# Performance work log

Hardware: AMD Instinct MI355X
Metric: run time of the kernel (lower is better)

## Reference

```python
import jax, jax.numpy as jnp
import numpy as np

N, B, LMAX, M, D, KV, H = 12288, 4, 4096, 1024, 256, 512, 8
EPS = 1e-5


def layernorm(x, g, b):
    mu = jnp.mean(x, axis=-1, keepdims=True)
    var = jnp.mean(jnp.square(x - mu), axis=-1, keepdims=True)
    return (x - mu) * jax.lax.rsqrt(var + EPS) * g + b


def setup_inputs() -> dict:
    key = jax.random.key(0)
    ks = jax.random.split(key, 8)
    s = 0.02
    F = jax.random.normal(ks[0], (N, D), jnp.float32)
    batch_idx = jnp.sort(jax.random.randint(ks[1], (N,), 0, B, dtype=jnp.int32))
    y = jax.random.normal(ks[2], (B, M, KV), jnp.float32)
    Wq = jax.random.normal(ks[3], (D, D), jnp.float32) * s
    Wk = jax.random.normal(ks[4], (D, KV), jnp.float32) * s
    Wv = jax.random.normal(ks[5], (D, KV), jnp.float32) * s
    Wo = jax.random.normal(ks[6], (D, D), jnp.float32) * s
    zb = jnp.zeros((D,), jnp.float32)
    return dict(F=F, batch_idx=batch_idx, y=y,
                Wq=Wq, bq=zb, Wk=Wk, bk=zb, Wv=Wv, bv=zb, Wo=Wo, bo=zb,
                ln_g=jnp.ones((D,), jnp.float32), ln_b=zb, Lmax=LMAX)


def reference(F, batch_idx, y, Wq, bq, Wk, bk, Wv, bv, Wo, bo, ln_g, ln_b, Lmax):
    Bn, Mn, _ = y.shape
    n, d = F.shape
    # sparse_to_dense: scatter points into [B, Lmax, D] by (batch, position-in-batch)
    counts = jax.ops.segment_sum(jnp.ones((n,), jnp.int32), batch_idx, num_segments=Bn)
    starts = jnp.cumsum(counts) - counts                      # first row of each batch
    pos = jnp.arange(n, dtype=jnp.int32) - starts[batch_idx]  # intra-batch position
    xd = jnp.zeros((Bn, Lmax, d), F.dtype).at[batch_idx, pos].set(F)
    # pre-norm (shared LayerNorm params, reused again post-residual)
    q_in = layernorm(xd, ln_g, ln_b)
    # multi-head cross-attention (no key padding mask: mask arg is None here)
    dh = d // H
    q = (q_in @ Wq.T + bq).reshape(Bn, Lmax, H, dh)
    k = (y @ Wk.T + bk).reshape(Bn, Mn, H, dh)
    v = (y @ Wv.T + bv).reshape(Bn, Mn, H, dh)
    scores = jnp.einsum('blhd,bmhd->bhlm', q, k) / jnp.sqrt(jnp.float32(dh))
    p = jax.nn.softmax(scores, axis=-1)
    o = jnp.einsum('bhlm,bmhd->blhd', p, v).reshape(Bn, Lmax, d)
    attn = o @ Wo.T + bo
    # residual on the (normed) query, then the SAME LayerNorm again
    res = layernorm(q_in + attn, ln_g, ln_b)
    # dense_to_sparse: gather valid rows back (row-major order == input order)
    return res[batch_idx, pos]
```

## Files before the change

### kernel.cpp

```cpp
#include <hip/hip_runtime.h>

constexpr int NP = 12288;
constexpr int NB = 4;
constexpr int MC = 1024;
constexpr int DM = 256;
constexpr int KVD = 512;
constexpr int NH = 8;
constexpr int DH = 32;

typedef __bf16 bf16x8 __attribute__((ext_vector_type(8)));
typedef __bf16 bf16x4 __attribute__((ext_vector_type(4)));
typedef float f32x4v __attribute__((ext_vector_type(4)));

__device__ inline bf16x8 pack8(float4 a, float4 b) {
    bf16x8 r;
    r[0] = (__bf16)a.x; r[1] = (__bf16)a.y; r[2] = (__bf16)a.z; r[3] = (__bf16)a.w;
    r[4] = (__bf16)b.x; r[5] = (__bf16)b.y; r[6] = (__bf16)b.z; r[7] = (__bf16)b.w;
    return r;
}

__global__ __launch_bounds__(256) void k_prep(const float* __restrict__ F,
        const int* __restrict__ bidx,
        const float* __restrict__ wq, const float* __restrict__ wk,
        const float* __restrict__ wv, const float* __restrict__ wo,
        const float* __restrict__ g, const float* __restrict__ bb,
        int* __restrict__ starts,
        __bf16* wqb, __bf16* wkb, __bf16* wvb, __bf16* wob,
        __bf16* __restrict__ q_in_b) {
    const int bid = blockIdx.x, t = threadIdx.x;
    if (bid == 0) {
        if (t > NB) return;
        int lo = 0, hi = NP;
        while (lo < hi) { int mid = (lo + hi) >> 1; if (bidx[mid] < t) lo = mid + 1; else hi = mid; }
        starts[t] = lo;
        return;
    }
    if (bid <= 384) {
        size_t i = ((size_t)(bid - 1) * 256 + t) * 4;
        const float* s; __bf16* d; size_t off;
        if      (i < 65536)  { s = wq; d = wqb; off = 0; }
        else if (i < 196608) { s = wk; d = wkb; off = 65536; }
        else if (i < 327680) { s = wv; d = wvb; off = 196608; }
        else                 { s = wo; d = wob; off = 327680; }
        size_t j = i - off;
        float4 v = *(const float4*)&s[j];
        bf16x4 o; o[0] = (__bf16)v.x; o[1] = (__bf16)v.y; o[2] = (__bf16)v.z; o[3] = (__bf16)v.w;
        *(bf16x4*)&d[j] = o;
        return;
    }
    const int w = t >> 6, l = t & 63;
    size_t row = (size_t)(bid - 385) * 4 + w;
    float4 v = *(const float4*)&F[row * DM + l * 4];
    float s = v.x + v.y + v.z + v.w;
#pragma unroll
    for (int o2 = 1; o2 < 64; o2 <<= 1) s += __shfl_xor(s, o2);
    float mu = s * (1.f / DM);
    float4 d = {v.x - mu, v.y - mu, v.z - mu, v.w - mu};
    float ss = d.x * d.x + d.y * d.y + d.z * d.z + d.w * d.w;
#pragma unroll
    for (int o2 = 1; o2 < 64; o2 <<= 1) ss += __shfl_xor(ss, o2);
    float rr = rsqrtf(ss * (1.f / DM) + 1e-5f);
    float4 gg = *(const float4*)&g[l * 4];
    float4 bv = *(const float4*)&bb[l * 4];
    bf16x4 ob4;
    ob4[0] = (__bf16)(d.x * rr * gg.x + bv.x);
    ob4[1] = (__bf16)(d.y * rr * gg.y + bv.y);
    ob4[2] = (__bf16)(d.z * rr * gg.z + bv.z);
    ob4[3] = (__bf16)(d.w * rr * gg.w + bv.w);
    *(bf16x4*)&q_in_b[row * DM + l * 4] = ob4;
}

__global__ __launch_bounds__(256) void k_qkv(const __bf16* __restrict__ Aq,
        const __bf16* __restrict__ Wq, const float* __restrict__ bq,
        const float* __restrict__ Yf,
        const __bf16* __restrict__ Wk, const float* __restrict__ bk,
        const __bf16* __restrict__ Wv, const float* __restrict__ bv,
        __bf16* __restrict__ Qo, __bf16* __restrict__ Kp,
        __bf16* __restrict__ VpT, float qscale) {
    __shared__ __bf16 As[128][68];
    __shared__ __bf16 Bs[64][68];
    const int t = threadIdx.x;
    const int w = t >> 6, l = t & 63, lg = l >> 4, ln = l & 15;
    const int wr = w >> 1, wc = w & 1;
    const int ar = t >> 3, ac8 = (t & 7) * 8;
    if ((int)blockIdx.x < 384) {
        f32x4v acc[4][2] = {};
        const int K = DM;
        const int col0 = (blockIdx.x & 3) * 64, row0 = (blockIdx.x >> 2) * 128;
        bf16x8 ra0, ra1, ra2, ra3, rb0, rb1;
#define LOADGQ(K0) \
        ra0 = *(const bf16x8*)&Aq[(size_t)(row0 + ar) * K + (K0) + ac8];        \
        ra1 = *(const bf16x8*)&Aq[(size_t)(row0 + ar + 32) * K + (K0) + ac8];   \
        ra2 = *(const bf16x8*)&Aq[(size_t)(row0 + ar + 64) * K + (K0) + ac8];   \
        ra3 = *(const bf16x8*)&Aq[(size_t)(row0 + ar + 96) * K + (K0) + ac8];   \
        rb0 = *(const bf16x8*)&Wq[(size_t)(col0 + ar) * K + (K0) + ac8];        \
        rb1 = *(const bf16x8*)&Wq[(size_t)(col0 + ar + 32) * K + (K0) + ac8];
        LOADGQ(0)
        for (int k0 = 0; k0 < K; k0 += 64) {
            __syncthreads();
            *(bf16x8*)&As[ar][ac8] = ra0;
            *(bf16x8*)&As[ar + 32][ac8] = ra1;
            *(bf16x8*)&As[ar + 64][ac8] = ra2;
            *(bf16x8*)&As[ar + 96][ac8] = ra3;
            *(bf16x8*)&Bs[ar][ac8] = rb0;
            *(bf16x8*)&Bs[ar + 32][ac8] = rb1;
            __syncthreads();
            if (k0 + 64 < K) { LOADGQ(k0 + 64) }
#pragma unroll
            for (int kk = 0; kk < 2; ++kk) {
                bf16x8 bfr[2];
#pragma unroll
                for (int ni = 0; ni < 2; ++ni) {
                    bf16x4 lo = *(const bf16x4*)&Bs[wc * 32 + ni * 16 + ln][kk * 32 + lg * 4];
                    bf16x4 hi = *(const bf16x4*)&Bs[wc * 32 + ni * 16 + ln][kk * 32 + 16 + lg * 4];
                    bfr[ni] = __builtin_shufflevector(lo, hi, 0, 1, 2, 3, 4, 5, 6, 7);
                }
#pragma unroll
                for (int mi = 0; mi < 4; ++mi) {
                    bf16x4 lo = *(const bf16x4*)&As[wr * 64 + mi * 16 + ln][kk * 32 + lg * 4];
                    bf16x4 hi = *(const bf16x4*)&As[wr * 64 + mi * 16 + ln][kk * 32 + 16 + lg * 4];
                    bf16x8 af = __builtin_shufflevector(lo, hi, 0, 1, 2, 3, 4, 5, 6, 7);
#pragma unroll
                    for (int ni = 0; ni < 2; ++ni)
                        acc[mi][ni] = __builtin_amdgcn_mfma_f32_16x16x32_bf16(bfr[ni], af, acc[mi][ni], 0, 0, 0);
                }
            }
        }
#undef LOADGQ
#pragma unroll
        for (int mi = 0; mi < 4; ++mi)
#pragma unroll
            for (int ni = 0; ni < 2; ++ni) {
                int cb = col0 + wc * 32 + ni * 16 + 4 * lg;
                float4 b4 = *(const float4*)&bq[cb];
                size_t row = row0 + wr * 64 + mi * 16 + ln;
                bf16x4 pk;
                pk[0] = (__bf16)((acc[mi][ni][0] + b4.x) * qscale);
                pk[1] = (__bf16)((acc[mi][ni][1] + b4.y) * qscale);
                pk[2] = (__bf16)((acc[mi][ni][2] + b4.z) * qscale);
                pk[3] = (__bf16)((acc[mi][ni][3] + b4.w) * qscale);
                *(bf16x4*)&Qo[row * DM + cb] = pk;
            }
    } else {
        f32x4v acc[2][2] = {};
        const int K = KVD;
        const int idx = blockIdx.x - 384;
        const int bx = idx & 7, row0 = (idx >> 3) * 64;
        const bool vpath = bx >= 4;
        const int col0 = (bx & 3) * 64;
        const __bf16* Wm = vpath ? Wv : Wk;
        const float* bi = vpath ? bv : bk;
        float4 a0, a1, a2, a3;
        bf16x8 rb0, rb1;
#define LOADGK(K0) \
        a0 = *(const float4*)&Yf[(size_t)(row0 + ar) * K + (K0) + ac8];            \
        a1 = *(const float4*)&Yf[(size_t)(row0 + ar) * K + (K0) + ac8 + 4];        \
        a2 = *(const float4*)&Yf[(size_t)(row0 + ar + 32) * K + (K0) + ac8];       \
        a3 = *(const float4*)&Yf[(size_t)(row0 + ar + 32) * K + (K0) + ac8 + 4];   \
        rb0 = *(const bf16x8*)&Wm[(size_t)(col0 + ar) * K + (K0) + ac8];           \
        rb1 = *(const bf16x8*)&Wm[(size_t)(col0 + ar + 32) * K + (K0) + ac8];
        LOADGK(0)
        for (int k0 = 0; k0 < K; k0 += 64) {
            __syncthreads();
            *(bf16x8*)&As[ar][ac8] = pack8(a0, a1);
            *(bf16x8*)&As[ar + 32][ac8] = pack8(a2, a3);
            *(bf16x8*)&Bs[ar][ac8] = rb0;
            *(bf16x8*)&Bs[ar + 32][ac8] = rb1;
            __syncthreads();
            if (k0 + 64 < K) { LOADGK(k0 + 64) }
#pragma unroll
            for (int kk = 0; kk < 2; ++kk) {
                bf16x8 bfr[2];
#pragma unroll
                for (int ni = 0; ni < 2; ++ni) {
                    bf16x4 lo = *(const bf16x4*)&Bs[wc * 32 + ni * 16 + ln][kk * 32 + lg * 4];
                    bf16x4 hi = *(const bf16x4*)&Bs[wc * 32 + ni * 16 + ln][kk * 32 + 16 + lg * 4];
                    bfr[ni] = __builtin_shufflevector(lo, hi, 0, 1, 2, 3, 4, 5, 6, 7);
                }
#pragma unroll
                for (int mi = 0; mi < 2; ++mi) {
                    bf16x4 lo = *(const bf16x4*)&As[wr * 32 + mi * 16 + ln][kk * 32 + lg * 4];
                    bf16x4 hi = *(const bf16x4*)&As[wr * 32 + mi * 16 + ln][kk * 32 + 16 + lg * 4];
                    bf16x8 af = __builtin_shufflevector(lo, hi, 0, 1, 2, 3, 4, 5, 6, 7);
#pragma unroll
                    for (int ni = 0; ni < 2; ++ni) {
                        if (vpath)
                            acc[mi][ni] = __builtin_amdgcn_mfma_f32_16x16x32_bf16(af, bfr[ni], acc[mi][ni], 0, 0, 0);
                        else
                            acc[mi][ni] = __builtin_amdgcn_mfma_f32_16x16x32_bf16(bfr[ni], af, acc[mi][ni], 0, 0, 0);
                    }
                }
            }
        }
#undef LOADGK
        if (vpath) {
#pragma unroll
            for (int mi = 0; mi < 2; ++mi)
#pragma unroll
                for (int ni = 0; ni < 2; ++ni) {
                    int col = col0 + wc * 32 + ni * 16 + ln;
                    float bvv = bi[col];
                    int grow = row0 + wr * 32 + mi * 16 + 4 * lg;
                    int b = grow >> 10, m = grow & 1023;
                    bf16x4 pk;
#pragma unroll
                    for (int r = 0; r < 4; ++r) pk[r] = (__bf16)(acc[mi][ni][r] + bvv);
                    *(bf16x4*)&VpT[((size_t)b * DM + col) * MC + m] = pk;
                }
        } else {
#pragma unroll
            for (int mi = 0; mi < 2; ++mi)
#pragma unroll
                for (int ni = 0; ni < 2; ++ni) {
                    int cb = col0 + wc * 32 + ni * 16 + 4 * lg;
                    float4 b4 = *(const float4*)&bi[cb];
                    size_t row = row0 + wr * 32 + mi * 16 + ln;
                    bf16x4 pk;
                    pk[0] = (__bf16)(acc[mi][ni][0] + b4.x);
                    pk[1] = (__bf16)(acc[mi][ni][1] + b4.y);
                    pk[2] = (__bf16)(acc[mi][ni][2] + b4.z);
                    pk[3] = (__bf16)(acc[mi][ni][3] + b4.w);
                    *(bf16x4*)&Kp[row * DM + cb] = pk;
                }
        }
    }
}

__global__ __launch_bounds__(256) void k_attn_mfma(const __bf16* __restrict__ q,
        const __bf16* __restrict__ Kc, const __bf16* __restrict__ VcT,
        const int* __restrict__ starts, __bf16* __restrict__ o) {
    const int b = blockIdx.z, h = blockIdx.y;
    const int r0 = starts[b] + blockIdx.x * 128;
    const int rend = starts[b + 1];
    if (r0 >= rend) return;
    const int nr = min(128, rend - r0);

    __shared__ __bf16 Ks[128][36];
    __shared__ __bf16 Vt[32][132];

    const int t = threadIdx.x;
    const int w = t >> 6, l = t & 63, lg = l >> 4, ln = l & 15;

    const __bf16* Kb = Kc + (size_t)b * MC * DM + h * DH;
    const __bf16* Vb = VcT + ((size_t)b * DM + h * DH) * MC;

    const int qr0 = min(r0 + w * 32 + ln, NP - 1);
    const int qr1 = min(r0 + w * 32 + 16 + ln, NP - 1);
    const __bf16* qp0 = q + (size_t)qr0 * DM + h * DH;
    const __bf16* qp1 = q + (size_t)qr1 * DM + h * DH;
    bf16x8 qf0 = __builtin_shufflevector(*(const bf16x4*)(qp0 + lg * 4),
                                         *(const bf16x4*)(qp0 + 16 + lg * 4),
                                         0, 1, 2, 3, 4, 5, 6, 7);
    bf16x8 qf1 = __builtin_shufflevector(*(const bf16x4*)(qp1 + lg * 4),
                                         *(const bf16x4*)(qp1 + 16 + lg * 4),
                                         0, 1, 2, 3, 4, 5, 6, 7);

    f32x4v OaccA[2] = {{0.f, 0.f, 0.f, 0.f}, {0.f, 0.f, 0.f, 0.f}};
    f32x4v OaccB[2] = {{0.f, 0.f, 0.f, 0.f}, {0.f, 0.f, 0.f, 0.f}};
    float lsA = 0.f, lsB = 0.f;

    const int kr = t >> 2, kc8 = (t & 3) * 8;
    const int vr = t >> 4, vc8 = (t & 15) * 8;

    bf16x8 rk0, rk1, rv0, rv1;
    rk0 = *(const bf16x8*)&Kb[(size_t)kr * DM + kc8];
    rk1 = *(const bf16x8*)&Kb[(size_t)(64 + kr) * DM + kc8];
    rv0 = *(const bf16x8*)&Vb[(size_t)vr * MC + vc8];
    rv1 = *(const bf16x8*)&Vb[(size_t)(16 + vr) * MC + vc8];

    for (int mt = 0; mt < 8; ++mt) {
        __syncthreads();
        *(bf16x8*)&Ks[kr][kc8] = rk0;
        *(bf16x8*)&Ks[64 + kr][kc8] = rk1;
        *(bf16x8*)&Vt[vr][vc8] = rv0;
        *(bf16x8*)&Vt[16 + vr][vc8] = rv1;
        __syncthreads();
        if (mt < 7) {
            const int m0 = (mt + 1) * 128;
            rk0 = *(const bf16x8*)&Kb[(size_t)(m0 + kr) * DM + kc8];
            rk1 = *(const bf16x8*)&Kb[(size_t)(m0 + 64 + kr) * DM + kc8];
            rv0 = *(const bf16x8*)&Vb[(size_t)vr * MC + m0 + vc8];
            rv1 = *(const bf16x8*)&Vb[(size_t)(16 + vr) * MC + m0 + vc8];
        }

        f32x4v S0[8], S1[8];
        __builtin_amdgcn_s_setprio(1);
#pragma unroll
        for (int ms = 0; ms < 8; ++ms) {
            bf16x4 lo = *(const bf16x4*)&Ks[ms * 16 + ln][lg * 4];
            bf16x4 hi = *(const bf16x4*)&Ks[ms * 16 + ln][16 + lg * 4];
            bf16x8 kf = __builtin_shufflevector(lo, hi, 0, 1, 2, 3, 4, 5, 6, 7);
            S0[ms] = __builtin_amdgcn_mfma_f32_16x16x32_bf16(
                kf, qf0, (f32x4v){0.f, 0.f, 0.f, 0.f}, 0, 0, 0);
            S1[ms] = __builtin_amdgcn_mfma_f32_16x16x32_bf16(
                kf, qf1, (f32x4v){0.f, 0.f, 0.f, 0.f}, 0, 0, 0);
        }
        __builtin_amdgcn_s_setprio(0);
        bf16x8 pa0[4], pa1[4];
#pragma unroll
        for (int ms = 0; ms < 8; ++ms) {
            const int mh = ms >> 1, j0 = (ms & 1) * 4;
#pragma unroll
            for (int r = 0; r < 4; ++r) {
                float e = __builtin_amdgcn_exp2f(S0[ms][r]);
                lsA += e;
                pa0[mh][j0 + r] = (__bf16)e;
            }
#pragma unroll
            for (int r = 0; r < 4; ++r) {
                float e = __builtin_amdgcn_exp2f(S1[ms][r]);
                lsB += e;
                pa1[mh][j0 + r] = (__bf16)e;
            }
        }
        __builtin_amdgcn_s_setprio(1);
#pragma unroll
        for (int mh = 0; mh < 4; ++mh)
#pragma unroll
            for (int nt = 0; nt < 2; ++nt) {
                bf16x4 lo = *(const bf16x4*)&Vt[nt * 16 + ln][mh * 32 + lg * 4];
                bf16x4 hi = *(const bf16x4*)&Vt[nt * 16 + ln][mh * 32 + 16 + lg * 4];
                bf16x8 vf = __builtin_shufflevector(lo, hi, 0, 1, 2, 3, 4, 5, 6, 7);
                OaccA[nt] = __builtin_amdgcn_mfma_f32_16x16x32_bf16(pa0[mh], vf, OaccA[nt], 0, 0, 0);
                OaccB[nt] = __builtin_amdgcn_mfma_f32_16x16x32_bf16(pa1[mh], vf, OaccB[nt], 0, 0, 0);
            }
        __builtin_amdgcn_s_setprio(0);
    }
    lsA += __shfl_xor(lsA, 16); lsA += __shfl_xor(lsA, 32);
    lsB += __shfl_xor(lsB, 16); lsB += __shfl_xor(lsB, 32);
    float invA = 1.0f / lsA, invB = 1.0f / lsB;
    float ivA[4], ivB[4];
#pragma unroll
    for (int r = 0; r < 4; ++r) {
        ivA[r] = __shfl(invA, 4 * lg + r);
        ivB[r] = __shfl(invB, 4 * lg + r);
    }
#pragma unroll
    for (int r = 0; r < 4; ++r) {
        int rlocA = w * 32 + 4 * lg + r;
        if (rlocA < nr) {
            size_t base = (size_t)(r0 + rlocA) * DM + h * DH + ln;
            o[base] = (__bf16)(OaccA[0][r] * ivA[r]);
            o[base + 16] = (__bf16)(OaccA[1][r] * ivA[r]);
        }
        int rlocB = w * 32 + 16 + 4 * lg + r;
        if (rlocB < nr) {
            size_t base = (size_t)(r0 + rlocB) * DM + h * DH + ln;
            o[base] = (__bf16)(OaccB[0][r] * ivB[r]);
            o[base + 16] = (__bf16)(OaccB[1][r] * ivB[r]);
        }
    }
}

__global__ __launch_bounds__(256) void k_gemmo_ln(const __bf16* __restrict__ A,
        const __bf16* __restrict__ W, const float* __restrict__ bias,
        const __bf16* __restrict__ resid, const float* __restrict__ g,
        const float* __restrict__ bb, float* __restrict__ out) {
    __shared__ __bf16 As[32][68];
    __shared__ __bf16 Bs[256][68];
    __shared__ float red[32][4][2];
    const int t = threadIdx.x;
    const int w = t >> 6, l = t & 63, lg = l >> 4, ln = l & 15;
    const int row0 = blockIdx.x * 32;
    const int ar = t >> 3, ac8 = (t & 7) * 8;
    f32x4v acc[2][4] = {};
    for (int k0 = 0; k0 < DM; k0 += 64) {
        __syncthreads();
        *(bf16x8*)&As[ar][ac8] = *(const bf16x8*)&A[(size_t)(row0 + ar) * DM + k0 + ac8];
#pragma unroll
        for (int j = 0; j < 8; ++j)
            *(bf16x8*)&Bs[ar + 32 * j][ac8] = *(const bf16x8*)&W[(size_t)(ar + 32 * j) * DM + k0 + ac8];
        __syncthreads();
#pragma unroll
        for (int kk = 0; kk < 2; ++kk) {
            bf16x8 bfr[4];
#pragma unroll
            for (int ni = 0; ni < 4; ++ni) {
                bf16x4 lo = *(const bf16x4*)&Bs[w * 64 + ni * 16 + ln][kk * 32 + lg * 4];
                bf16x4 hi = *(const bf16x4*)&Bs[w * 64 + ni * 16 + ln][kk * 32 + 16 + lg * 4];
                bfr[ni] = __builtin_shufflevector(lo, hi, 0, 1, 2, 3, 4, 5, 6, 7);
            }
#pragma unroll
            for (int mi = 0; mi < 2; ++mi) {
                bf16x4 lo = *(const bf16x4*)&As[mi * 16 + ln][kk * 32 + lg * 4];
                bf16x4 hi = *(const bf16x4*)&As[mi * 16 + ln][kk * 32 + 16 + lg * 4];
                bf16x8 af = __builtin_shufflevector(lo, hi, 0, 1, 2, 3, 4, 5, 6, 7);
#pragma unroll
                for (int ni = 0; ni < 4; ++ni)
                    acc[mi][ni] = __builtin_amdgcn_mfma_f32_16x16x32_bf16(bfr[ni], af, acc[mi][ni], 0, 0, 0);
            }
        }
    }
    float s[2] = {0.f, 0.f}, ss[2] = {0.f, 0.f};
#pragma unroll
    for (int mi = 0; mi < 2; ++mi) {
        int row = row0 + mi * 16 + ln;
#pragma unroll
        for (int ni = 0; ni < 4; ++ni) {
            int cb = w * 64 + ni * 16 + lg * 4;
            float4 b4 = *(const float4*)&bias[cb];
            bf16x4 rv = *(const bf16x4*)&resid[(size_t)row * DM + cb];
            float z0 = acc[mi][ni][0] + b4.x + (float)rv[0];
            float z1 = acc[mi][ni][1] + b4.y + (float)rv[1];
            float z2 = acc[mi][ni][2] + b4.z + (float)rv[2];
            float z3 = acc[mi][ni][3] + b4.w + (float)rv[3];
            acc[mi][ni][0] = z0; acc[mi][ni][1] = z1;
            acc[mi][ni][2] = z2; acc[mi][ni][3] = z3;
            s[mi] += (z0 + z1) + (z2 + z3);
            ss[mi] += (z0 * z0 + z1 * z1) + (z2 * z2 + z3 * z3);
        }
    }
#pragma unroll
    for (int mi = 0; mi < 2; ++mi) {
        s[mi] += __shfl_xor(s[mi], 16);  s[mi] += __shfl_xor(s[mi], 32);
        ss[mi] += __shfl_xor(ss[mi], 16); ss[mi] += __shfl_xor(ss[mi], 32);
    }
    if (l < 16) {
#pragma unroll
        for (int mi = 0; mi < 2; ++mi) {
            red[mi * 16 + ln][w][0] = s[mi];
            red[mi * 16 + ln][w][1] = ss[mi];
        }
    }
    __syncthreads();
#pragma unroll
    for (int mi = 0; mi < 2; ++mi) {
        int rloc = mi * 16 + ln;
        float su = (red[rloc][0][0] + red[rloc][1][0]) + (red[rloc][2][0] + red[rloc][3][0]);
        float sq = (red[rloc][0][1] + red[rloc][1][1]) + (red[rloc][2][1] + red[rloc][3][1]);
        float mu = su * (1.f / DM);
        float var = sq * (1.f / DM) - mu * mu;
        float rs = rsqrtf(var + 1e-5f);
        size_t row = row0 + rloc;
#pragma unroll
        for (int ni = 0; ni < 4; ++ni) {
            int cb = w * 64 + ni * 16 + lg * 4;
            float4 g4 = *(const float4*)&g[cb];
            float4 bb4 = *(const float4*)&bb[cb];
            float4 o4;
            o4.x = (acc[mi][ni][0] - mu) * rs * g4.x + bb4.x;
            o4.y = (acc[mi][ni][1] - mu) * rs * g4.y + bb4.y;
            o4.z = (acc[mi][ni][2] - mu) * rs * g4.z + bb4.z;
            o4.w = (acc[mi][ni][3] - mu) * rs * g4.w + bb4.w;
            *(float4*)&out[row * DM + cb] = o4;
        }
    }
}

extern "C" void kernel_launch(void* const* d_in, const int* in_sizes, int n_in,
                              void* d_out, int out_size, void* d_ws, size_t ws_size,
                              hipStream_t stream) {
    const float* F  = (const float*)d_in[0];
    const int* bidx = (const int*)d_in[1];
    const float* y  = (const float*)d_in[2];
    const float* Wq = (const float*)d_in[3];
    const float* bq = (const float*)d_in[4];
    const float* Wk = (const float*)d_in[5];
    const float* bk = (const float*)d_in[6];
    const float* Wv = (const float*)d_in[7];
    const float* bv = (const float*)d_in[8];
    const float* Wo = (const float*)d_in[9];
    const float* bo = (const float*)d_in[10];
    const float* lg = (const float*)d_in[11];
    const float* lb = (const float*)d_in[12];
    float* out = (float*)d_out;

    char* ws = (char*)d_ws;
    __bf16* q_in_b = (__bf16*)ws;   ws += (size_t)NP * DM * 2;
    __bf16* qb     = (__bf16*)ws;   ws += (size_t)NP * DM * 2;
    __bf16* ob     = (__bf16*)ws;   ws += (size_t)NP * DM * 2;
    __bf16* Kp     = (__bf16*)ws;   ws += (size_t)NB * MC * DM * 2;
    __bf16* VpT    = (__bf16*)ws;   ws += (size_t)NB * DM * MC * 2;
    __bf16* Wq_b   = (__bf16*)ws;   ws += (size_t)DM * DM * 2;
    __bf16* Wk_b   = (__bf16*)ws;   ws += (size_t)DM * KVD * 2;
    __bf16* Wv_b   = (__bf16*)ws;   ws += (size_t)DM * KVD * 2;
    __bf16* Wo_b   = (__bf16*)ws;   ws += (size_t)DM * DM * 2;
    int* starts    = (int*)ws;

    const float qscale = 0.17677669529663687f * 1.4426950408889634f;

    k_prep<<<1 + 384 + NP / 4, 256, 0, stream>>>(F, bidx, Wq, Wk, Wv, Wo, lg, lb,
            starts, Wq_b, Wk_b, Wv_b, Wo_b, q_in_b);
    k_qkv<<<384 + 512, 256, 0, stream>>>(q_in_b, Wq_b, bq, y, Wk_b, bk, Wv_b, bv,
            qb, Kp, VpT, qscale);
    k_attn_mfma<<<dim3(NP / 128, NH, NB), 256, 0, stream>>>(qb, Kp, VpT, starts, ob);
    k_gemmo_ln<<<NP / 32, 256, 0, stream>>>(ob, Wo_b, bo, q_in_b, lg, lb, out);
}
```

Baseline: 71.45 us.

## Store K/V in MFMA fragment order and load fragments directly from global

```diff
diff --git a/kernel.cpp b/kernel.cpp
--- a/kernel.cpp
+++ b/kernel.cpp
@@ -75,8 +75,8 @@
         const float* __restrict__ Yf,
         const __bf16* __restrict__ Wk, const float* __restrict__ bk,
         const __bf16* __restrict__ Wv, const float* __restrict__ bv,
-        __bf16* __restrict__ Qo, __bf16* __restrict__ Kp,
-        __bf16* __restrict__ VpT, float qscale) {
+        __bf16* __restrict__ Qo, __bf16* __restrict__ Kf,
+        __bf16* __restrict__ Vf, float qscale) {
     __shared__ __bf16 As[128][68];
     __shared__ __bf16 Bs[64][68];
     const int t = threadIdx.x;
@@ -194,40 +194,47 @@
         }
 #undef LOADGK
         if (vpath) {
+            const int h = (col0 + wc * 32) >> 5;
 #pragma unroll
             for (int mi = 0; mi < 2; ++mi)
 #pragma unroll
                 for (int ni = 0; ni < 2; ++ni) {
-                    int col = col0 + wc * 32 + ni * 16 + ln;
-                    float bvv = bi[col];
-                    int grow = row0 + wr * 32 + mi * 16 + 4 * lg;
-                    int b = grow >> 10, m = grow & 1023;
+                    int C = col0 + wc * 32 + ni * 16 + ln;
+                    int nt = (C >> 4) & 1;
+                    float bvv = bi[C];
+                    int m = row0 + wr * 32 + mi * 16 + 4 * lg;
+                    int b = m >> 10, mlocal = m & 1023;
+                    int mhg = mlocal >> 5;
                     bf16x4 pk;
 #pragma unroll
                     for (int r = 0; r < 4; ++r) pk[r] = (__bf16)(acc[mi][ni][r] + bvv);
-                    *(bf16x4*)&VpT[((size_t)b * DM + col) * MC + m] = pk;
+                    *(bf16x4*)&Vf[(size_t)(((b * NH + h) * 32 + mhg) * 2 + nt) * 512 + l * 8 + mi * 4] = pk;
                 }
         } else {
-#pragma unroll
-            for (int mi = 0; mi < 2; ++mi)
+            const int h = (col0 + wc * 32) >> 5;
+#pragma unroll
+            for (int mi = 0; mi < 2; ++mi) {
+                int m = row0 + wr * 32 + mi * 16 + ln;
+                int b = m >> 10, mlocal = m & 1023;
+                int msg = mlocal >> 4;
 #pragma unroll
                 for (int ni = 0; ni < 2; ++ni) {
                     int cb = col0 + wc * 32 + ni * 16 + 4 * lg;
                     float4 b4 = *(const float4*)&bi[cb];
-                    size_t row = row0 + wr * 32 + mi * 16 + ln;
                     bf16x4 pk;
                     pk[0] = (__bf16)(acc[mi][ni][0] + b4.x);
                     pk[1] = (__bf16)(acc[mi][ni][1] + b4.y);
                     pk[2] = (__bf16)(acc[mi][ni][2] + b4.z);
                     pk[3] = (__bf16)(acc[mi][ni][3] + b4.w);
-                    *(bf16x4*)&Kp[row * DM + cb] = pk;
-                }
+                    *(bf16x4*)&Kf[(size_t)((b * NH + h) * 64 + msg) * 512 + l * 8 + ni * 4] = pk;
+                }
+            }
         }
     }
 }
 
 __global__ __launch_bounds__(256) void k_attn_mfma(const __bf16* __restrict__ q,
-        const __bf16* __restrict__ Kc, const __bf16* __restrict__ VcT,
+        const __bf16* __restrict__ Kf, const __bf16* __restrict__ Vf,
         const int* __restrict__ starts, __bf16* __restrict__ o) {
     const int b = blockIdx.z, h = blockIdx.y;
     const int r0 = starts[b] + blockIdx.x * 128;
@@ -235,14 +242,11 @@
     if (r0 >= rend) return;
     const int nr = min(128, rend - r0);
 
-    __shared__ __bf16 Ks[128][36];
-    __shared__ __bf16 Vt[32][132];
-
     const int t = threadIdx.x;
     const int w = t >> 6, l = t & 63, lg = l >> 4, ln = l & 15;
 
-    const __bf16* Kb = Kc + (size_t)b * MC * DM + h * DH;
-    const __bf16* Vb = VcT + ((size_t)b * DM + h * DH) * MC;
+    const __bf16* kfb = Kf + (size_t)(b * NH + h) * 32768;
+    const __bf16* vfb = Vf + (size_t)(b * NH + h) * 32768;
 
     const int qr0 = min(r0 + w * 32 + ln, NP - 1);
     const int qr1 = min(r0 + w * 32 + 16 + ln, NP - 1);
@@ -257,45 +261,28 @@
 
     f32x4v OaccA[2] = {{0.f, 0.f, 0.f, 0.f}, {0.f, 0.f, 0.f, 0.f}};
     f32x4v OaccB[2] = {{0.f, 0.f, 0.f, 0.f}, {0.f, 0.f, 0.f, 0.f}};
-    float lsA = 0.f, lsB = 0.f;
-
-    const int kr = t >> 2, kc8 = (t & 3) * 8;
-    const int vr = t >> 4, vc8 = (t & 15) * 8;
-
-    bf16x8 rk0, rk1, rv0, rv1;
-    rk0 = *(const bf16x8*)&Kb[(size_t)kr * DM + kc8];
-    rk1 = *(const bf16x8*)&Kb[(size_t)(64 + kr) * DM + kc8];
-    rv0 = *(const bf16x8*)&Vb[(size_t)vr * MC + vc8];
-    rv1 = *(const bf16x8*)&Vb[(size_t)(16 + vr) * MC + vc8];
+    float lsA4[4] = {0.f, 0.f, 0.f, 0.f};
+    float lsB4[4] = {0.f, 0.f, 0.f, 0.f};
 
     for (int mt = 0; mt < 8; ++mt) {
-        __syncthreads();
-        *(bf16x8*)&Ks[kr][kc8] = rk0;
-        *(bf16x8*)&Ks[64 + kr][kc8] = rk1;
-        *(bf16x8*)&Vt[vr][vc8] = rv0;
-        *(bf16x8*)&Vt[16 + vr][vc8] = rv1;
-        __syncthreads();
-        if (mt < 7) {
-            const int m0 = (mt + 1) * 128;
-            rk0 = *(const bf16x8*)&Kb[(size_t)(m0 + kr) * DM + kc8];
-            rk1 = *(const bf16x8*)&Kb[(size_t)(m0 + 64 + kr) * DM + kc8];
-            rv0 = *(const bf16x8*)&Vb[(size_t)vr * MC + m0 + vc8];
-            rv1 = *(const bf16x8*)&Vb[(size_t)(16 + vr) * MC + m0 + vc8];
-        }
-
+        bf16x8 kfr[8];
+#pragma unroll
+        for (int ms = 0; ms < 8; ++ms)
+            kfr[ms] = *(const bf16x8*)&kfb[(size_t)((mt * 8 + ms) * 64 + l) * 8];
         f32x4v S0[8], S1[8];
         __builtin_amdgcn_s_setprio(1);
 #pragma unroll
         for (int ms = 0; ms < 8; ++ms) {
-            bf16x4 lo = *(const bf16x4*)&Ks[ms * 16 + ln][lg * 4];
-            bf16x4 hi = *(const bf16x4*)&Ks[ms * 16 + ln][16 + lg * 4];
-            bf16x8 kf = __builtin_shufflevector(lo, hi, 0, 1, 2, 3, 4, 5, 6, 7);
             S0[ms] = __builtin_amdgcn_mfma_f32_16x16x32_bf16(
-                kf, qf0, (f32x4v){0.f, 0.f, 0.f, 0.f}, 0, 0, 0);
+                kfr[ms], qf0, (f32x4v){0.f, 0.f, 0.f, 0.f}, 0, 0, 0);
             S1[ms] = __builtin_amdgcn_mfma_f32_16x16x32_bf16(
-                kf, qf1, (f32x4v){0.f, 0.f, 0.f, 0.f}, 0, 0, 0);
+                kfr[ms], qf1, (f32x4v){0.f, 0.f, 0.f, 0.f}, 0, 0, 0);
         }
         __builtin_amdgcn_s_setprio(0);
+        bf16x8 vfr[8];
+#pragma unroll
+        for (int i = 0; i < 8; ++i)
+            vfr[i] = *(const bf16x8*)&vfb[(size_t)((mt * 8 + i) * 64 + l) * 8];
         bf16x8 pa0[4], pa1[4];
 #pragma unroll
         for (int ms = 0; ms < 8; ++ms) {
@@ -303,13 +290,13 @@
 #pragma unroll
             for (int r = 0; r < 4; ++r) {
                 float e = __builtin_amdgcn_exp2f(S0[ms][r]);
-                lsA += e;
+                lsA4[r] += e;
                 pa0[mh][j0 + r] = (__bf16)e;
             }
 #pragma unroll
             for (int r = 0; r < 4; ++r) {
                 float e = __builtin_amdgcn_exp2f(S1[ms][r]);
-                lsB += e;
+                lsB4[r] += e;
                 pa1[mh][j0 + r] = (__bf16)e;
             }
         }
@@ -318,14 +305,13 @@
         for (int mh = 0; mh < 4; ++mh)
 #pragma unroll
             for (int nt = 0; nt < 2; ++nt) {
-                bf16x4 lo = *(const bf16x4*)&Vt[nt * 16 + ln][mh * 32 + lg * 4];
-                bf16x4 hi = *(const bf16x4*)&Vt[nt * 16 + ln][mh * 32 + 16 + lg * 4];
-                bf16x8 vf = __builtin_shufflevector(lo, hi, 0, 1, 2, 3, 4, 5, 6, 7);
-                OaccA[nt] = __builtin_amdgcn_mfma_f32_16x16x32_bf16(pa0[mh], vf, OaccA[nt], 0, 0, 0);
-                OaccB[nt] = __builtin_amdgcn_mfma_f32_16x16x32_bf16(pa1[mh], vf, OaccB[nt], 0, 0, 0);
+                OaccA[nt] = __builtin_amdgcn_mfma_f32_16x16x32_bf16(pa0[mh], vfr[mh * 2 + nt], OaccA[nt], 0, 0, 0);
+                OaccB[nt] = __builtin_amdgcn_mfma_f32_16x16x32_bf16(pa1[mh], vfr[mh * 2 + nt], OaccB[nt], 0, 0, 0);
             }
         __builtin_amdgcn_s_setprio(0);
     }
+    float lsA = (lsA4[0] + lsA4[1]) + (lsA4[2] + lsA4[3]);
+    float lsB = (lsB4[0] + lsB4[1]) + (lsB4[2] + lsB4[3]);
     lsA += __shfl_xor(lsA, 16); lsA += __shfl_xor(lsA, 32);
     lsB += __shfl_xor(lsB, 16); lsB += __shfl_xor(lsB, 32);
     float invA = 1.0f / lsA, invB = 1.0f / lsB;
@@ -469,8 +455,8 @@
     __bf16* q_in_b = (__bf16*)ws;   ws += (size_t)NP * DM * 2;
     __bf16* qb     = (__bf16*)ws;   ws += (size_t)NP * DM * 2;
     __bf16* ob     = (__bf16*)ws;   ws += (size_t)NP * DM * 2;
-    __bf16* Kp     = (__bf16*)ws;   ws += (size_t)NB * MC * DM * 2;
-    __bf16* VpT    = (__bf16*)ws;   ws += (size_t)NB * DM * MC * 2;
+    __bf16* Kf     = (__bf16*)ws;   ws += (size_t)NB * MC * DM * 2;
+    __bf16* Vf     = (__bf16*)ws;   ws += (size_t)NB * DM * MC * 2;
     __bf16* Wq_b   = (__bf16*)ws;   ws += (size_t)DM * DM * 2;
     __bf16* Wk_b   = (__bf16*)ws;   ws += (size_t)DM * KVD * 2;
     __bf16* Wv_b   = (__bf16*)ws;   ws += (size_t)DM * KVD * 2;
@@ -482,7 +468,7 @@
     k_prep<<<1 + 384 + NP / 4, 256, 0, stream>>>(F, bidx, Wq, Wk, Wv, Wo, lg, lb,
             starts, Wq_b, Wk_b, Wv_b, Wo_b, q_in_b);
     k_qkv<<<384 + 512, 256, 0, stream>>>(q_in_b, Wq_b, bq, y, Wk_b, bk, Wv_b, bv,
-            qb, Kp, VpT, qscale);
-    k_attn_mfma<<<dim3(NP / 128, NH, NB), 256, 0, stream>>>(qb, Kp, VpT, starts, ob);
+            qb, Kf, Vf, qscale);
+    k_attn_mfma<<<dim3(NP / 128, NH, NB), 256, 0, stream>>>(qb, Kf, Vf, starts, ob);
     k_gemmo_ln<<<NP / 32, 256, 0, stream>>>(ob, Wo_b, bo, q_in_b, lg, lb, out);
 }
```

Result: no change. 70.70 us (-1.1%).
